# Performance work log

Measured on AMD Instinct MI355X. Metric: run time of the kernel, lower is better.

Reference implementation:

```python
import jax, jax.numpy as jnp
import numpy as np

N = 8192
IN_F = 128
N_HID = 64
OUT_F = 128
NEG = -9.0e15


def _xavier(key, shape, gain=1.414):
    fan_in, fan_out = shape
    a = gain * np.sqrt(6.0 / (fan_in + fan_out))
    return jax.random.uniform(key, shape, jnp.float32, -a, a)


def setup_inputs() -> dict:
    key = jax.random.key(0)
    k_h, k_adj, k_ws, k_wt, k_wc = jax.random.split(key, 5)
    h = jax.random.normal(k_h, (N, IN_F), dtype=jnp.float32)
    adj = jax.random.randint(k_adj, (N, N), 0, 2, dtype=jnp.int32)
    Ws = _xavier(k_ws, (IN_F, N_HID))
    Wt = _xavier(k_wt, (IN_F, N_HID))
    Wc = _xavier(k_wc, (IN_F, OUT_F))
    return {"h": h, "adj": adj, "Ws": Ws, "Wt": Wt, "Wc": Wc}


def reference(h, adj, Ws, Wt, Wc):
    # Whs: [N, H], Wht: [N, H]
    Whs = h @ Ws
    Wht = h @ Wt
    # e: [N, N] dense attention scores
    e = jnp.einsum("nh,mh->nm", Whs, Wht)
    z = jnp.where(adj > 0, e, jnp.asarray(NEG, e.dtype))
    alpha = jax.nn.softmax(z, axis=-1)  # [N, N]
    Whc = h @ Wc                        # [N, OUT_F]
    h_prime = alpha @ Whc               # [N, OUT_F]
    return h_prime
```

## Files before the change

### kernel.cpp

```cpp
#include <hip/hip_runtime.h>


#define NN 8192
#define INF_ 128
#define NHID 64
#define OUTF 128
#define NEGC -9.0e15f

typedef unsigned short u16;
typedef __attribute__((ext_vector_type(8))) short bf16x8;
typedef __attribute__((ext_vector_type(4))) float f32x4;
typedef __attribute__((ext_vector_type(4))) int i32x4;
typedef __attribute__((ext_vector_type(4))) unsigned u32x4;

static __device__ __forceinline__ u16 f2bf(float x) {
  union { float f; unsigned u; } v; v.f = x;
  unsigned lsb = (v.u >> 16) & 1u;
  v.u += 0x7fffu + lsb;
  return (u16)(v.u >> 16);
}
static __device__ __forceinline__ float bf2f(u16 h) {
  union { float f; unsigned u; } v; v.u = ((unsigned)h) << 16;
  return v.f;
}
static __device__ __forceinline__ f32x4 mfma16(bf16x8 a, bf16x8 b, f32x4 c) {
  return __builtin_amdgcn_mfma_f32_16x16x32_bf16(a, b, c, 0, 0, 0);
}

__global__ __launch_bounds__(256) void proj_kernel(
    const float* __restrict__ h, const float* __restrict__ Ws,
    const float* __restrict__ Wt, const float* __restrict__ Wc,
    u16* __restrict__ whs_hi, u16* __restrict__ whs_lo,
    u16* __restrict__ wht_hi, u16* __restrict__ wht_lo,
    u16* __restrict__ whcT) {
  __shared__ f32x4 hbuf[8][32];
  const int tid = threadIdx.x;
  const int r0 = blockIdx.x * 8;
  hbuf[tid >> 5][tid & 31] =
      reinterpret_cast<const f32x4*>(h)[(size_t)r0 * 32 + tid];
  __syncthreads();

  float acc[8];
#pragma unroll
  for (int r = 0; r < 8; ++r) acc[r] = 0.f;

  if (tid < 128) {
    const float* W = (tid < 64) ? (Ws + tid) : (Wt + (tid - 64));
#pragma unroll 4
    for (int k4 = 0; k4 < 32; ++k4) {
      float w0 = W[(k4 * 4 + 0) * NHID];
      float w1 = W[(k4 * 4 + 1) * NHID];
      float w2 = W[(k4 * 4 + 2) * NHID];
      float w3 = W[(k4 * 4 + 3) * NHID];
#pragma unroll
      for (int r = 0; r < 8; ++r) {
        f32x4 hv = hbuf[r][k4];
        acc[r] += hv.x * w0 + hv.y * w1 + hv.z * w2 + hv.w * w3;
      }
    }
    const int col = tid & 63;
    const float sc = (tid < 64) ? 1.4426950408889634f : 1.0f;
    u16* hi = (tid < 64) ? whs_hi : wht_hi;
    u16* lo = (tid < 64) ? whs_lo : wht_lo;
#pragma unroll
    for (int r = 0; r < 8; ++r) {
      float v = acc[r] * sc;
      u16 hb = f2bf(v);
      hi[(size_t)(r0 + r) * NHID + col] = hb;
      lo[(size_t)(r0 + r) * NHID + col] = f2bf(v - bf2f(hb));
    }
  } else {
    const int col = tid - 128;
    const float* W = Wc + col;
#pragma unroll 4
    for (int k4 = 0; k4 < 32; ++k4) {
      float w0 = W[(k4 * 4 + 0) * OUTF];
      float w1 = W[(k4 * 4 + 1) * OUTF];
      float w2 = W[(k4 * 4 + 2) * OUTF];
      float w3 = W[(k4 * 4 + 3) * OUTF];
#pragma unroll
      for (int r = 0; r < 8; ++r) {
        f32x4 hv = hbuf[r][k4];
        acc[r] += hv.x * w0 + hv.y * w1 + hv.z * w2 + hv.w * w3;
      }
    }
    union { u16 s[8]; u32x4 v; } pk;
#pragma unroll
    for (int r = 0; r < 8; ++r) pk.s[r] = f2bf(acc[r]);
    *reinterpret_cast<u32x4*>(whcT + (size_t)col * NN + r0) = pk.v;
  }
}

__global__ __launch_bounds__(256, 2) void attn_kernel(
    const u16* __restrict__ whs_hi, const u16* __restrict__ whs_lo,
    const u16* __restrict__ wht_hi, const u16* __restrict__ wht_lo,
    const u16* __restrict__ whcT, const int* __restrict__ adj,
    float* __restrict__ Opart, float* __restrict__ mpart,
    float* __restrict__ lpart, float* __restrict__ out,
    int iters, int cshift, int final_write) {
  __shared__ __align__(16) u16 Bst[2][2][64 * 72];
  __shared__ __align__(16) u16 Wst[2][128 * 64];
  __shared__ __align__(16) u16 Pbuf[4][16][72];
  __shared__ __align__(16) u16 Mbuf[2][64][4];

  const int tid = threadIdx.x;
  const int w = tid >> 6;
  const int lane = tid & 63;
  const int q = lane >> 4;
  const int ln = lane & 15;
  const int chunk = blockIdx.x & ((1 << cshift) - 1);
  const int rb = blockIdx.x >> cshift;
  const int rowB = rb * 64;
  const int row0 = rowB + w * 16;

  const int bcol = tid >> 2;
  const int bsh = (tid >> 1) & 1;
  const int bkh = tid & 1;
  const u16* bg = (bsh ? wht_lo : wht_hi) + (size_t)bcol * NHID + bkh * 32;
  const int wocol = tid >> 1;
  const int wjh = tid & 1;
  const u16* wg = whcT + (size_t)wocol * NN + wjh * 32;
  int wsp[4];
#pragma unroll
  for (int i = 0; i < 4; ++i) wsp[i] = ((wjh * 4 + i + wocol) & 7) * 8;
  const int arow = tid >> 2;
  const int agrp = tid & 3;
  const int* ag = adj + (size_t)(rowB + arow) * NN + agrp * 16;

  bf16x8 a_hi[2], a_lo[2];
#pragma unroll
  for (int kh = 0; kh < 2; ++kh) {
    a_hi[kh] = *reinterpret_cast<const bf16x8*>(
        whs_hi + (size_t)(row0 + ln) * NHID + kh * 32 + q * 8);
    a_lo[kh] = *reinterpret_cast<const bf16x8*>(
        whs_lo + (size_t)(row0 + ln) * NHID + kh * 32 + q * 8);
  }

  f32x4 oacc[8];
#pragma unroll
  for (int ot = 0; ot < 8; ++ot)
#pragma unroll
    for (int g = 0; g < 4; ++g) oacc[ot][g] = 0.f;

  float m_old = -__builtin_inff();
  float l_run = 0.f;

  const int jbase = chunk * iters;

  {
    const size_t j0 = (size_t)jbase * 64;
    const u32x4* p = reinterpret_cast<const u32x4*>(bg + j0 * NHID);
    u32x4 b0 = p[0], b1 = p[1], b2 = p[2], b3 = p[3];
    const u32x4* pw = reinterpret_cast<const u32x4*>(wg + j0);
    u32x4 w0 = pw[0], w1 = pw[1], w2 = pw[2], w3 = pw[3];
    const i32x4* pa = reinterpret_cast<const i32x4*>(ag + j0);
    i32x4 a0 = __builtin_nontemporal_load(pa + 0);
    i32x4 a1 = __builtin_nontemporal_load(pa + 1);
    i32x4 a2 = __builtin_nontemporal_load(pa + 2);
    i32x4 a3 = __builtin_nontemporal_load(pa + 3);
    u32x4* d = reinterpret_cast<u32x4*>(&Bst[0][bsh][bcol * 72 + bkh * 32]);
    d[0] = b0; d[1] = b1; d[2] = b2; d[3] = b3;
    *reinterpret_cast<u32x4*>(&Wst[0][wocol * 64 + wsp[0]]) = w0;
    *reinterpret_cast<u32x4*>(&Wst[0][wocol * 64 + wsp[1]]) = w1;
    *reinterpret_cast<u32x4*>(&Wst[0][wocol * 64 + wsp[2]]) = w2;
    *reinterpret_cast<u32x4*>(&Wst[0][wocol * 64 + wsp[3]]) = w3;
    unsigned mw = 0;
    mw |= (a0.x>0?1u:0u)<<0  | (a0.y>0?1u:0u)<<1  | (a0.z>0?1u:0u)<<2  | (a0.w>0?1u:0u)<<3;
    mw |= (a1.x>0?1u:0u)<<4  | (a1.y>0?1u:0u)<<5  | (a1.z>0?1u:0u)<<6  | (a1.w>0?1u:0u)<<7;
    mw |= (a2.x>0?1u:0u)<<8  | (a2.y>0?1u:0u)<<9  | (a2.z>0?1u:0u)<<10 | (a2.w>0?1u:0u)<<11;
    mw |= (a3.x>0?1u:0u)<<12 | (a3.y>0?1u:0u)<<13 | (a3.z>0?1u:0u)<<14 | (a3.w>0?1u:0u)<<15;
    Mbuf[0][arow][agrp] = (u16)mw;
  }
  __syncthreads();

  for (int jt = 0; jt < iters; ++jt) {
    const int buf = jt & 1;

    u32x4 sb0, sb1, sb2, sb3, sw0, sw1, sw2, sw3;
    i32x4 ad0, ad1, ad2, ad3;
    if (jt + 1 < iters) {
      const size_t j1 = (size_t)(jbase + jt + 1) * 64;
      const u32x4* p = reinterpret_cast<const u32x4*>(bg + j1 * NHID);
      sb0 = p[0]; sb1 = p[1]; sb2 = p[2]; sb3 = p[3];
      const u32x4* pw = reinterpret_cast<const u32x4*>(wg + j1);
      sw0 = pw[0]; sw1 = pw[1]; sw2 = pw[2]; sw3 = pw[3];
      const i32x4* pa = reinterpret_cast<const i32x4*>(ag + j1);
      ad0 = __builtin_nontemporal_load(pa + 0);
      ad1 = __builtin_nontemporal_load(pa + 1);
      ad2 = __builtin_nontemporal_load(pa + 2);
      ad3 = __builtin_nontemporal_load(pa + 3);
    }

    const unsigned* mrow =
        reinterpret_cast<const unsigned*>(&Mbuf[buf][w * 16 + ln][0]);
    const unsigned m0 = mrow[0];
    const unsigned m1 = mrow[1];

    const u16* Bh = &Bst[buf][0][0];
    const u16* Bl = &Bst[buf][1][0];
    float s[4][4];
#pragma unroll
    for (int nt = 0; nt < 4; ++nt) {
      const int base = (nt * 16 + ln) * 72 + q * 8;
      bf16x8 bh0 = *reinterpret_cast<const bf16x8*>(&Bh[base]);
      bf16x8 bh1 = *reinterpret_cast<const bf16x8*>(&Bh[base + 32]);
      bf16x8 bl0 = *reinterpret_cast<const bf16x8*>(&Bl[base]);
      bf16x8 bl1 = *reinterpret_cast<const bf16x8*>(&Bl[base + 32]);
      f32x4 sa;
#pragma unroll
      for (int g = 0; g < 4; ++g) sa[g] = 0.f;
      sa = mfma16(bh0, a_lo[0], sa);
      sa = mfma16(bl0, a_hi[0], sa);
      sa = mfma16(bh0, a_hi[0], sa);
      sa = mfma16(bh1, a_lo[1], sa);
      sa = mfma16(bl1, a_hi[1], sa);
      sa = mfma16(bh1, a_hi[1], sa);
      const unsigned mm = (nt & 2) ? m1 : m0;
#pragma unroll
      for (int g = 0; g < 4; ++g) {
        unsigned bit = (mm >> ((nt & 1) * 16 + q * 4 + g)) & 1u;
        s[nt][g] = bit ? sa[g] : NEGC;
      }
    }

    float rmax;
    {
      float t0 = fmaxf(fmaxf(s[0][0], s[0][1]), fmaxf(s[0][2], s[0][3]));
      float t1 = fmaxf(fmaxf(s[1][0], s[1][1]), fmaxf(s[1][2], s[1][3]));
      float t2 = fmaxf(fmaxf(s[2][0], s[2][1]), fmaxf(s[2][2], s[2][3]));
      float t3 = fmaxf(fmaxf(s[3][0], s[3][1]), fmaxf(s[3][2], s[3][3]));
      rmax = fmaxf(fmaxf(t0, t1), fmaxf(t2, t3));
    }
    rmax = fmaxf(rmax, __shfl_xor(rmax, 16));
    rmax = fmaxf(rmax, __shfl_xor(rmax, 32));

    if (__any(rmax > m_old)) {
      const float mn = fmaxf(m_old, rmax);
      const float al = __builtin_amdgcn_exp2f(m_old - mn);
      m_old = mn;
      l_run *= al;
      float alg[4];
#pragma unroll
      for (int g = 0; g < 4; ++g) alg[g] = __shfl(al, q * 4 + g);
#pragma unroll
      for (int ot = 0; ot < 8; ++ot)
#pragma unroll
        for (int g = 0; g < 4; ++g) oacc[ot][g] *= alg[g];
    }

    float ps = 0.f;
#pragma unroll
    for (int nt = 0; nt < 4; ++nt) {
      float p0 = __builtin_amdgcn_exp2f(s[nt][0] - m_old);
      float p1 = __builtin_amdgcn_exp2f(s[nt][1] - m_old);
      float p2 = __builtin_amdgcn_exp2f(s[nt][2] - m_old);
      float p3 = __builtin_amdgcn_exp2f(s[nt][3] - m_old);
      ps += (p0 + p1) + (p2 + p3);
      union { u16 h[4]; unsigned long long u; } pk;
      pk.h[0] = f2bf(p0); pk.h[1] = f2bf(p1);
      pk.h[2] = f2bf(p2); pk.h[3] = f2bf(p3);
      *reinterpret_cast<unsigned long long*>(
          &Pbuf[w][ln][nt * 16 + q * 4]) = pk.u;
    }
    ps += __shfl_xor(ps, 16);
    ps += __shfl_xor(ps, 32);
    l_run += ps;

#pragma unroll
    for (int kh = 0; kh < 2; ++kh) {
      bf16x8 pa = *reinterpret_cast<const bf16x8*>(
          &Pbuf[w][ln][kh * 32 + q * 8]);
      const int pp = ((kh << 2) + q + ln) & 7;
#pragma unroll
      for (int ot = 0; ot < 8; ++ot) {
        const int ocol = ot * 16 + ln;
        bf16x8 wb = *reinterpret_cast<const bf16x8*>(
            &Wst[buf][ocol * 64 + pp * 8]);
        oacc[ot] = mfma16(pa, wb, oacc[ot]);
      }
    }

    if (jt + 1 < iters) {
      const int nb = buf ^ 1;
      u32x4* d = reinterpret_cast<u32x4*>(&Bst[nb][bsh][bcol * 72 + bkh * 32]);
      d[0] = sb0; d[1] = sb1; d[2] = sb2; d[3] = sb3;
      *reinterpret_cast<u32x4*>(&Wst[nb][wocol * 64 + wsp[0]]) = sw0;
      *reinterpret_cast<u32x4*>(&Wst[nb][wocol * 64 + wsp[1]]) = sw1;
      *reinterpret_cast<u32x4*>(&Wst[nb][wocol * 64 + wsp[2]]) = sw2;
      *reinterpret_cast<u32x4*>(&Wst[nb][wocol * 64 + wsp[3]]) = sw3;
      unsigned mw = 0;
      mw |= (ad0.x>0?1u:0u)<<0  | (ad0.y>0?1u:0u)<<1  | (ad0.z>0?1u:0u)<<2  | (ad0.w>0?1u:0u)<<3;
      mw |= (ad1.x>0?1u:0u)<<4  | (ad1.y>0?1u:0u)<<5  | (ad1.z>0?1u:0u)<<6  | (ad1.w>0?1u:0u)<<7;
      mw |= (ad2.x>0?1u:0u)<<8  | (ad2.y>0?1u:0u)<<9  | (ad2.z>0?1u:0u)<<10 | (ad2.w>0?1u:0u)<<11;
      mw |= (ad3.x>0?1u:0u)<<12 | (ad3.y>0?1u:0u)<<13 | (ad3.z>0?1u:0u)<<14 | (ad3.w>0?1u:0u)<<15;
      Mbuf[buf ^ 1][arow][agrp] = (u16)mw;
    }
    __syncthreads();
  }

  if (final_write) {
    float lr[4];
#pragma unroll
    for (int g = 0; g < 4; ++g) lr[g] = __shfl(l_run, q * 4 + g);
#pragma unroll
    for (int ot = 0; ot < 8; ++ot)
#pragma unroll
      for (int g = 0; g < 4; ++g) {
        const int r = row0 + q * 4 + g;
        out[(size_t)r * OUTF + ot * 16 + ln] = oacc[ot][g] / lr[g];
      }
  } else {
#pragma unroll
    for (int ot = 0; ot < 8; ++ot)
#pragma unroll
      for (int g = 0; g < 4; ++g) {
        const int r = row0 + q * 4 + g;
        Opart[((size_t)chunk * NN + r) * OUTF + ot * 16 + ln] = oacc[ot][g];
      }
    if (lane < 16) {
      mpart[chunk * NN + row0 + ln] = m_old;
      lpart[chunk * NN + row0 + ln] = l_run;
    }
  }
}

__global__ __launch_bounds__(256) void combine_kernel(
    const float* __restrict__ Opart, const float* __restrict__ mpart,
    const float* __restrict__ lpart, float* __restrict__ out, int C) {
  const int idx = blockIdx.x * 256 + threadIdx.x;
  const int row = idx >> 7;
  float M = -__builtin_inff();
  for (int c = 0; c < C; ++c) M = fmaxf(M, mpart[c * NN + row]);
  float den = 0.f, num = 0.f;
  for (int c = 0; c < C; ++c) {
    float wgt = __builtin_amdgcn_exp2f(mpart[c * NN + row] - M);
    den += lpart[c * NN + row] * wgt;
    num += Opart[(size_t)c * NN * OUTF + idx] * wgt;
  }
  out[idx] = num / den;
}

extern "C" void kernel_launch(void* const* d_in, const int* in_sizes, int n_in,
                              void* d_out, int out_size, void* d_ws, size_t ws_size,
                              hipStream_t stream) {
  const float* h   = (const float*)d_in[0];
  const int*   adj = (const int*)d_in[1];
  const float* Ws  = (const float*)d_in[2];
  const float* Wt  = (const float*)d_in[3];
  const float* Wc  = (const float*)d_in[4];
  float* out = (float*)d_out;

  char* ws = (char*)d_ws;
  const size_t MB = 1024 * 1024;
  u16* whs_hi = (u16*)(ws);
  u16* whs_lo = (u16*)(ws + 1 * MB);
  u16* wht_hi = (u16*)(ws + 2 * MB);
  u16* wht_lo = (u16*)(ws + 3 * MB);
  u16* whcT   = (u16*)(ws + 4 * MB);
  float* mpart = (float*)(ws + 6 * MB);
  float* lpart = (float*)(ws + 6 * MB + 256 * 1024);
  float* Opart = (float*)(ws + 6 * MB + 512 * 1024);

  int C = 4, cshift = 2;
  if (6 * MB + 512 * 1024 + (size_t)C * NN * OUTF * sizeof(float) > ws_size) {
    C = 1; cshift = 0;
  }
  const int final_write = (C == 1) ? 1 : 0;
  const int iters = NN / (C * 64);

  proj_kernel<<<NN / 8, 256, 0, stream>>>(h, Ws, Wt, Wc, whs_hi, whs_lo,
                                          wht_hi, wht_lo, whcT);
  attn_kernel<<<(NN / 64) * C, 256, 0, stream>>>(
      whs_hi, whs_lo, wht_hi, wht_lo, whcT, adj, Opart, mpart, lpart, out,
      iters, cshift, final_write);
  if (!final_write)
    combine_kernel<<<NN * OUTF / 256, 256, 0, stream>>>(Opart, mpart, lpart,
                                                        out, C);
}
```

Before: 440.5 us.

## Deepen global prefetch to two tiles ahead with a ping-pong register stage

The main loop is unrolled by two and split into issue, commit and compute lambdas. Global loads of B, W and adjacency for tile jt+2 are issued before computing tile jt, using two register staging sets. The aim is to hide more global-memory latency behind the MFMA and softmax work. The cost is a second register stage of twelve 128-bit vectors, which raises VGPR pressure and may reduce occupancy.

```diff
diff --git a/kernel.cpp b/kernel.cpp
--- a/kernel.cpp
+++ b/kernel.cpp
@@ -146,6 +146,132 @@
   float l_run = 0.f;
 
   const int jbase = chunk * iters;
+
+  struct Stage {
+    u32x4 b0, b1, b2, b3;
+    u32x4 w0, w1, w2, w3;
+    i32x4 a0, a1, a2, a3;
+  };
+  Stage SA, SB;
+
+  auto issue = [&](Stage& S, int jtile) {
+    const size_t j = (size_t)jtile * 64;
+    const u32x4* p = reinterpret_cast<const u32x4*>(bg + j * NHID);
+    S.b0 = p[0]; S.b1 = p[1]; S.b2 = p[2]; S.b3 = p[3];
+    const u32x4* pw = reinterpret_cast<const u32x4*>(wg + j);
+    S.w0 = pw[0]; S.w1 = pw[1]; S.w2 = pw[2]; S.w3 = pw[3];
+    const i32x4* pa = reinterpret_cast<const i32x4*>(ag + j);
+    S.a0 = __builtin_nontemporal_load(pa + 0);
+    S.a1 = __builtin_nontemporal_load(pa + 1);
+    S.a2 = __builtin_nontemporal_load(pa + 2);
+    S.a3 = __builtin_nontemporal_load(pa + 3);
+  };
+
+  auto commit = [&](int nb, const Stage& S) {
+    u32x4* d = reinterpret_cast<u32x4*>(&Bst[nb][bsh][bcol * 72 + bkh * 32]);
+    d[0] = S.b0; d[1] = S.b1; d[2] = S.b2; d[3] = S.b3;
+    *reinterpret_cast<u32x4*>(&Wst[nb][wocol * 64 + wsp[0]]) = S.w0;
+    *reinterpret_cast<u32x4*>(&Wst[nb][wocol * 64 + wsp[1]]) = S.w1;
+    *reinterpret_cast<u32x4*>(&Wst[nb][wocol * 64 + wsp[2]]) = S.w2;
+    *reinterpret_cast<u32x4*>(&Wst[nb][wocol * 64 + wsp[3]]) = S.w3;
+    unsigned mw = 0;
+    mw |= (S.a0.x>0?1u:0u)<<0  | (S.a0.y>0?1u:0u)<<1  | (S.a0.z>0?1u:0u)<<2  | (S.a0.w>0?1u:0u)<<3;
+    mw |= (S.a1.x>0?1u:0u)<<4  | (S.a1.y>0?1u:0u)<<5  | (S.a1.z>0?1u:0u)<<6  | (S.a1.w>0?1u:0u)<<7;
+    mw |= (S.a2.x>0?1u:0u)<<8  | (S.a2.y>0?1u:0u)<<9  | (S.a2.z>0?1u:0u)<<10 | (S.a2.w>0?1u:0u)<<11;
+    mw |= (S.a3.x>0?1u:0u)<<12 | (S.a3.y>0?1u:0u)<<13 | (S.a3.z>0?1u:0u)<<14 | (S.a3.w>0?1u:0u)<<15;
+    Mbuf[nb][arow][agrp] = (u16)mw;
+  };
+
+  auto compute = [&](int buf) {
+    const unsigned* mrow =
+        reinterpret_cast<const unsigned*>(&Mbuf[buf][w * 16 + ln][0]);
+    const unsigned m0 = mrow[0];
+    const unsigned m1 = mrow[1];
+
+    const u16* Bh = &Bst[buf][0][0];
+    const u16* Bl = &Bst[buf][1][0];
+    float s[4][4];
+#pragma unroll
+    for (int nt = 0; nt < 4; ++nt) {
+      const int base = (nt * 16 + ln) * 72 + q * 8;
+      bf16x8 bh0 = *reinterpret_cast<const bf16x8*>(&Bh[base]);
+      bf16x8 bh1 = *reinterpret_cast<const bf16x8*>(&Bh[base + 32]);
+      bf16x8 bl0 = *reinterpret_cast<const bf16x8*>(&Bl[base]);
+      bf16x8 bl1 = *reinterpret_cast<const bf16x8*>(&Bl[base + 32]);
+      f32x4 sa;
+#pragma unroll
+      for (int g = 0; g < 4; ++g) sa[g] = 0.f;
+      sa = mfma16(bh0, a_lo[0], sa);
+      sa = mfma16(bl0, a_hi[0], sa);
+      sa = mfma16(bh0, a_hi[0], sa);
+      sa = mfma16(bh1, a_lo[1], sa);
+      sa = mfma16(bl1, a_hi[1], sa);
+      sa = mfma16(bh1, a_hi[1], sa);
+#pragma unroll
+      for (int g = 0; g < 4; ++g) {
+        const unsigned mm = (nt & 2) ? m1 : m0;
+        unsigned bit = (mm >> ((nt & 1) * 16 + q * 4 + g)) & 1u;
+        s[nt][g] = bit ? sa[g] : NEGC;
+      }
+    }
+
+    float rmax;
+    {
+      float t0 = fmaxf(fmaxf(s[0][0], s[0][1]), fmaxf(s[0][2], s[0][3]));
+      float t1 = fmaxf(fmaxf(s[1][0], s[1][1]), fmaxf(s[1][2], s[1][3]));
+      float t2 = fmaxf(fmaxf(s[2][0], s[2][1]), fmaxf(s[2][2], s[2][3]));
+      float t3 = fmaxf(fmaxf(s[3][0], s[3][1]), fmaxf(s[3][2], s[3][3]));
+      rmax = fmaxf(fmaxf(t0, t1), fmaxf(t2, t3));
+    }
+    rmax = fmaxf(rmax, __shfl_xor(rmax, 16));
+    rmax = fmaxf(rmax, __shfl_xor(rmax, 32));
+
+    if (__any(rmax > m_old)) {
+      const float mn = fmaxf(m_old, rmax);
+      const float al = __builtin_amdgcn_exp2f(m_old - mn);
+      m_old = mn;
+      l_run *= al;
+      float alg[4];
+#pragma unroll
+      for (int g = 0; g < 4; ++g) alg[g] = __shfl(al, q * 4 + g);
+#pragma unroll
+      for (int ot = 0; ot < 8; ++ot)
+#pragma unroll
+        for (int g = 0; g < 4; ++g) oacc[ot][g] *= alg[g];
+    }
+
+    float ps = 0.f;
+#pragma unroll
+    for (int nt = 0; nt < 4; ++nt) {
+      float p0 = __builtin_amdgcn_exp2f(s[nt][0] - m_old);
+      float p1 = __builtin_amdgcn_exp2f(s[nt][1] - m_old);
+      float p2 = __builtin_amdgcn_exp2f(s[nt][2] - m_old);
+      float p3 = __builtin_amdgcn_exp2f(s[nt][3] - m_old);
+      ps += (p0 + p1) + (p2 + p3);
+      union { u16 h[4]; unsigned long long u; } pk;
+      pk.h[0] = f2bf(p0); pk.h[1] = f2bf(p1);
+      pk.h[2] = f2bf(p2); pk.h[3] = f2bf(p3);
+      *reinterpret_cast<unsigned long long*>(
+          &Pbuf[w][ln][nt * 16 + q * 4]) = pk.u;
+    }
+    ps += __shfl_xor(ps, 16);
+    ps += __shfl_xor(ps, 32);
+    l_run += ps;
+
+#pragma unroll
+    for (int kh = 0; kh < 2; ++kh) {
+      bf16x8 pa = *reinterpret_cast<const bf16x8*>(
+          &Pbuf[w][ln][kh * 32 + q * 8]);
+#pragma unroll
+      for (int ot = 0; ot < 8; ++ot) {
+        const int ocol = ot * 16 + ln;
+        const int pp = ((kh << 2) + q + ocol) & 7;
+        bf16x8 wb = *reinterpret_cast<const bf16x8*>(
+            &Wst[buf][ocol * 64 + pp * 8]);
+        oacc[ot] = mfma16(pa, wb, oacc[ot]);
+      }
+    }
+  };
 
   {
     const size_t j0 = (size_t)jbase * 64;
@@ -171,130 +297,19 @@
     mw |= (a3.x>0?1u:0u)<<12 | (a3.y>0?1u:0u)<<13 | (a3.z>0?1u:0u)<<14 | (a3.w>0?1u:0u)<<15;
     Mbuf[0][arow][agrp] = (u16)mw;
   }
+  if (1 < iters) issue(SA, jbase + 1);
   __syncthreads();
 
-  for (int jt = 0; jt < iters; ++jt) {
-    const int buf = jt & 1;
-
-    u32x4 sb0, sb1, sb2, sb3, sw0, sw1, sw2, sw3;
-    i32x4 ad0, ad1, ad2, ad3;
-    if (jt + 1 < iters) {
-      const size_t j1 = (size_t)(jbase + jt + 1) * 64;
-      const u32x4* p = reinterpret_cast<const u32x4*>(bg + j1 * NHID);
-      sb0 = p[0]; sb1 = p[1]; sb2 = p[2]; sb3 = p[3];
-      const u32x4* pw = reinterpret_cast<const u32x4*>(wg + j1);
-      sw0 = pw[0]; sw1 = pw[1]; sw2 = pw[2]; sw3 = pw[3];
-      const i32x4* pa = reinterpret_cast<const i32x4*>(ag + j1);
-      ad0 = __builtin_nontemporal_load(pa + 0);
-      ad1 = __builtin_nontemporal_load(pa + 1);
-      ad2 = __builtin_nontemporal_load(pa + 2);
-      ad3 = __builtin_nontemporal_load(pa + 3);
-    }
-
-    const unsigned* mrow =
-        reinterpret_cast<const unsigned*>(&Mbuf[buf][w * 16 + ln][0]);
-    const unsigned m0 = mrow[0];
-    const unsigned m1 = mrow[1];
-
-    const u16* Bh = &Bst[buf][0][0];
-    const u16* Bl = &Bst[buf][1][0];
-    float s[4][4];
-#pragma unroll
-    for (int nt = 0; nt < 4; ++nt) {
-      const int base = (nt * 16 + ln) * 72 + q * 8;
-      bf16x8 bh0 = *reinterpret_cast<const bf16x8*>(&Bh[base]);
-      bf16x8 bh1 = *reinterpret_cast<const bf16x8*>(&Bh[base + 32]);
-      bf16x8 bl0 = *reinterpret_cast<const bf16x8*>(&Bl[base]);
-      bf16x8 bl1 = *reinterpret_cast<const bf16x8*>(&Bl[base + 32]);
-      f32x4 sa;
-#pragma unroll
-      for (int g = 0; g < 4; ++g) sa[g] = 0.f;
-      sa = mfma16(bh0, a_lo[0], sa);
-      sa = mfma16(bl0, a_hi[0], sa);
-      sa = mfma16(bh0, a_hi[0], sa);
-      sa = mfma16(bh1, a_lo[1], sa);
-      sa = mfma16(bl1, a_hi[1], sa);
-      sa = mfma16(bh1, a_hi[1], sa);
-      const unsigned mm = (nt & 2) ? m1 : m0;
-#pragma unroll
-      for (int g = 0; g < 4; ++g) {
-        unsigned bit = (mm >> ((nt & 1) * 16 + q * 4 + g)) & 1u;
-        s[nt][g] = bit ? sa[g] : NEGC;
-      }
-    }
-
-    float rmax;
-    {
-      float t0 = fmaxf(fmaxf(s[0][0], s[0][1]), fmaxf(s[0][2], s[0][3]));
-      float t1 = fmaxf(fmaxf(s[1][0], s[1][1]), fmaxf(s[1][2], s[1][3]));
-      float t2 = fmaxf(fmaxf(s[2][0], s[2][1]), fmaxf(s[2][2], s[2][3]));
-      float t3 = fmaxf(fmaxf(s[3][0], s[3][1]), fmaxf(s[3][2], s[3][3]));
-      rmax = fmaxf(fmaxf(t0, t1), fmaxf(t2, t3));
-    }
-    rmax = fmaxf(rmax, __shfl_xor(rmax, 16));
-    rmax = fmaxf(rmax, __shfl_xor(rmax, 32));
-
-    if (__any(rmax > m_old)) {
-      const float mn = fmaxf(m_old, rmax);
-      const float al = __builtin_amdgcn_exp2f(m_old - mn);
-      m_old = mn;
-      l_run *= al;
-      float alg[4];
-#pragma unroll
-      for (int g = 0; g < 4; ++g) alg[g] = __shfl(al, q * 4 + g);
-#pragma unroll
-      for (int ot = 0; ot < 8; ++ot)
-#pragma unroll
-        for (int g = 0; g < 4; ++g) oacc[ot][g] *= alg[g];
-    }
-
-    float ps = 0.f;
-#pragma unroll
-    for (int nt = 0; nt < 4; ++nt) {
-      float p0 = __builtin_amdgcn_exp2f(s[nt][0] - m_old);
-      float p1 = __builtin_amdgcn_exp2f(s[nt][1] - m_old);
-      float p2 = __builtin_amdgcn_exp2f(s[nt][2] - m_old);
-      float p3 = __builtin_amdgcn_exp2f(s[nt][3] - m_old);
-      ps += (p0 + p1) + (p2 + p3);
-      union { u16 h[4]; unsigned long long u; } pk;
-      pk.h[0] = f2bf(p0); pk.h[1] = f2bf(p1);
-      pk.h[2] = f2bf(p2); pk.h[3] = f2bf(p3);
-      *reinterpret_cast<unsigned long long*>(
-          &Pbuf[w][ln][nt * 16 + q * 4]) = pk.u;
-    }
-    ps += __shfl_xor(ps, 16);
-    ps += __shfl_xor(ps, 32);
-    l_run += ps;
-
-#pragma unroll
-    for (int kh = 0; kh < 2; ++kh) {
-      bf16x8 pa = *reinterpret_cast<const bf16x8*>(
-          &Pbuf[w][ln][kh * 32 + q * 8]);
-      const int pp = ((kh << 2) + q + ln) & 7;
-#pragma unroll
-      for (int ot = 0; ot < 8; ++ot) {
-        const int ocol = ot * 16 + ln;
-        bf16x8 wb = *reinterpret_cast<const bf16x8*>(
-            &Wst[buf][ocol * 64 + pp * 8]);
-        oacc[ot] = mfma16(pa, wb, oacc[ot]);
-      }
-    }
-
-    if (jt + 1 < iters) {
-      const int nb = buf ^ 1;
-      u32x4* d = reinterpret_cast<u32x4*>(&Bst[nb][bsh][bcol * 72 + bkh * 32]);
-      d[0] = sb0; d[1] = sb1; d[2] = sb2; d[3] = sb3;
-      *reinterpret_cast<u32x4*>(&Wst[nb][wocol * 64 + wsp[0]]) = sw0;
-      *reinterpret_cast<u32x4*>(&Wst[nb][wocol * 64 + wsp[1]]) = sw1;
-      *reinterpret_cast<u32x4*>(&Wst[nb][wocol * 64 + wsp[2]]) = sw2;
-      *reinterpret_cast<u32x4*>(&Wst[nb][wocol * 64 + wsp[3]]) = sw3;
-      unsigned mw = 0;
-      mw |= (ad0.x>0?1u:0u)<<0  | (ad0.y>0?1u:0u)<<1  | (ad0.z>0?1u:0u)<<2  | (ad0.w>0?1u:0u)<<3;
-      mw |= (ad1.x>0?1u:0u)<<4  | (ad1.y>0?1u:0u)<<5  | (ad1.z>0?1u:0u)<<6  | (ad1.w>0?1u:0u)<<7;
-      mw |= (ad2.x>0?1u:0u)<<8  | (ad2.y>0?1u:0u)<<9  | (ad2.z>0?1u:0u)<<10 | (ad2.w>0?1u:0u)<<11;
-      mw |= (ad3.x>0?1u:0u)<<12 | (ad3.y>0?1u:0u)<<13 | (ad3.z>0?1u:0u)<<14 | (ad3.w>0?1u:0u)<<15;
-      Mbuf[buf ^ 1][arow][agrp] = (u16)mw;
-    }
+  for (int jt = 0; jt < iters; jt += 2) {
+    if (jt + 2 < iters) issue(SB, jbase + jt + 2);
+    compute(0);
+    if (jt + 1 < iters) commit(1, SA);
+    __syncthreads();
+    if (jt + 1 >= iters) break;
+
+    if (jt + 3 < iters) issue(SA, jbase + jt + 3);
+    compute(1);
+    if (jt + 2 < iters) commit(0, SB);
     __syncthreads();
   }
 
```

Measured after the change: 464.4 us. 5.4% more time.
